# Performance work log

Measured on AMD Instinct MI355X. Metric: run time of the kernel, lower is better.

## Reference

```python
import jax, jax.numpy as jnp
import numpy as np

HIDDEN = 768
INTER = 2048
N_EXPERTS = 8
TOP_K = 2
SWIGLU_LIMIT = 7.0
N_TOK = 8192


def setup_inputs() -> dict:
    key = jax.random.key(0)
    k_x, k_r, k_gu, k_d = jax.random.split(key, 4)
    x = jax.random.normal(k_x, (N_TOK, HIDDEN), dtype=jnp.float32)
    router_w = jax.random.normal(k_r, (N_EXPERTS, HIDDEN), dtype=jnp.float32) * 0.02
    gate_up_proj = jax.random.normal(k_gu, (N_EXPERTS, 2 * INTER, HIDDEN), dtype=jnp.float32) * 0.02
    down_proj = jax.random.normal(k_d, (N_EXPERTS, HIDDEN, INTER), dtype=jnp.float32) * 0.02
    return {"x": x, "router_w": router_w, "gate_up_proj": gate_up_proj, "down_proj": down_proj}


def reference(x, router_w, gate_up_proj, down_proj):
    # router: [n_tok, E]
    router_logits = x @ router_w.T
    topk_vals, topk_idx = jax.lax.top_k(router_logits, TOP_K)  # [n_tok, k]
    topk_weights = jax.nn.softmax(topk_vals.astype(jnp.float32), axis=-1).astype(x.dtype)

    out = jnp.zeros_like(x)
    # Loop over the small fixed expert set; each expert is a dense GEMM over all
    # tokens, masked by its per-token routing weight (0 for unrouted tokens) —
    # identical math to the original gather/GEMM/scatter dispatch.
    for e in range(N_EXPERTS):
        # per-token weight for expert e (sums slots; each expert appears at most once per token)
        w_e = jnp.sum(jnp.where(topk_idx == e, topk_weights, 0.0), axis=-1)  # [n_tok]
        gate_up = x @ gate_up_proj[e].T  # [n_tok, 2*I]
        gate, up = jnp.split(gate_up, 2, axis=-1)
        up = jnp.minimum(up, SWIGLU_LIMIT)
        mlp_out = (jax.nn.silu(gate) * up) @ down_proj[e].T  # [n_tok, H]
        out = out + mlp_out * w_e[:, None]
    return out
```

## Files before the change

### kernel.cpp

```cpp
#include <hip/hip_runtime.h>
#include <hip/hip_bf16.h>

typedef unsigned short u16;
typedef unsigned int u32;
typedef short bf16x8 __attribute__((ext_vector_type(8)));
typedef float f32x4 __attribute__((ext_vector_type(4)));

#define NTOK 8192
#define HID 768
#define INTER 2048
#define NEXP 8

#define MFMA16(a, b, c) __builtin_amdgcn_mfma_f32_16x16x32_bf16(a, b, c, 0, 0, 0)
#define S_BARRIER() __builtin_amdgcn_s_barrier()
#define SETPRIO(x) __builtin_amdgcn_s_setprio(x)
#define WAITVM(n) asm volatile("s_waitcnt vmcnt(" #n ")" ::: "memory")

__device__ __forceinline__ u16 f2bf(float f) {
    u32 u = __builtin_bit_cast(u32, f);
    u32 r = (u + 0x7FFFu + ((u >> 16) & 1u)) >> 16;
    return (u16)r;
}

__device__ __forceinline__ void gld16(const void* g, void* l) {
    __builtin_amdgcn_global_load_lds((const __attribute__((address_space(1))) void*)g,
                                     (__attribute__((address_space(3))) void*)l, 16, 0, 0);
}

__global__ __launch_bounds__(256) void zero_kernel(float4* out4, int n4) {
    int i = blockIdx.x * blockDim.x + threadIdx.x;
    float4 z = {0.f, 0.f, 0.f, 0.f};
    int stride = gridDim.x * blockDim.x;
    for (int k = i; k < n4; k += stride) out4[k] = z;
}

__global__ __launch_bounds__(256) void cvt_kernel(const float* __restrict__ src, u16* __restrict__ dst, int n8) {
    int i = blockIdx.x * blockDim.x + threadIdx.x;
    int stride = gridDim.x * blockDim.x;
    for (; i < n8; i += stride) {
        const float4* s = (const float4*)(src + (size_t)i * 8);
        float4 a = s[0], b = s[1];
        u16 r[8] = {f2bf(a.x), f2bf(a.y), f2bf(a.z), f2bf(a.w),
                    f2bf(b.x), f2bf(b.y), f2bf(b.z), f2bf(b.w)};
        *(uint4*)(dst + (size_t)i * 8) = *(const uint4*)r;
    }
}

__global__ __launch_bounds__(256) void router2(const float* __restrict__ x, const float* __restrict__ rw,
                                               u32* __restrict__ route, float* __restrict__ wslot) {
    int wv = threadIdx.x >> 6, ln = threadIdx.x & 63;
    int t = blockIdx.x * 4 + wv;
    if (t >= NTOK) return;
    float xr[12];
#pragma unroll
    for (int j = 0; j < 12; j++) xr[j] = x[(size_t)t * HID + ln + j * 64];
    float lg[NEXP];
#pragma unroll
    for (int e = 0; e < NEXP; e++) {
        float a = 0.f;
#pragma unroll
        for (int j = 0; j < 12; j++) a += xr[j] * rw[e * HID + ln + j * 64];
#pragma unroll
        for (int off = 32; off; off >>= 1) a += __shfl_xor(a, off);
        lg[e] = a;
    }
    int i0 = 0;
    float v0 = lg[0];
#pragma unroll
    for (int e = 1; e < NEXP; e++)
        if (lg[e] > v0) { v0 = lg[e]; i0 = e; }
    int i1 = -1;
    float v1 = -1e30f;
#pragma unroll
    for (int e = 0; e < NEXP; e++) {
        if (e == i0) continue;
        if (lg[e] > v1) { v1 = lg[e]; i1 = e; }
    }
    float w0 = 1.f / (1.f + __expf(v1 - v0));
    float w1 = 1.f - w0;
    if (ln == 0) {
        wslot[0 * NTOK + t] = w0;
        wslot[1 * NTOK + t] = w1;
        route[t] = (u32)i0 | ((u32)i1 << 8);
    }
}

__global__ __launch_bounds__(1024) void scatter_kernel(const u32* __restrict__ route, int* __restrict__ counts,
                                                       int* __restrict__ tokslot, int* __restrict__ ntiles,
                                                       int* __restrict__ tiledesc) {
    __shared__ int sc[NEXP][1024];
    int tid = threadIdx.x;
    u32 rt[8];
    int cnt[NEXP] = {0, 0, 0, 0, 0, 0, 0, 0};
#pragma unroll
    for (int k = 0; k < 8; k++) {
        rt[k] = route[tid * 8 + k];
        cnt[rt[k] & 255]++;
        cnt[(rt[k] >> 8) & 255]++;
    }
#pragma unroll
    for (int e = 0; e < NEXP; e++) sc[e][tid] = cnt[e];
    __syncthreads();
    for (int off = 1; off < 1024; off <<= 1) {
        int v[NEXP];
#pragma unroll
        for (int e = 0; e < NEXP; e++) v[e] = (tid >= off) ? sc[e][tid - off] : 0;
        __syncthreads();
#pragma unroll
        for (int e = 0; e < NEXP; e++)
            if (tid >= off) sc[e][tid] += v[e];
        __syncthreads();
    }
    int base[NEXP];
#pragma unroll
    for (int e = 0; e < NEXP; e++) base[e] = sc[e][tid] - cnt[e];
#pragma unroll
    for (int k = 0; k < 8; k++) {
        int t = tid * 8 + k;
        int e0 = rt[k] & 255, e1 = (rt[k] >> 8) & 255;
        tokslot[e0 * NTOK + base[e0]] = t;
        base[e0]++;
        tokslot[e1 * NTOK + base[e1]] = t | (1 << 16);
        base[e1]++;
    }
    if (tid == 0) {
        int tot = 0;
        for (int e = 0; e < NEXP; e++) {
            int c = sc[e][1023];
            counts[e] = c;
            int nt = (c + 255) >> 8;
            for (int q = 0; q < nt; q++) tiledesc[tot++] = (e << 8) | q;
        }
        ntiles[0] = tot;
    }
}


#define STAGE4(d, kt)                                        \
    do {                                                     \
        char* dA_ = lds + (d)*32768 + tid * 16;              \
        char* dB_ = dA_ + 16384;                             \
        size_t ko_ = (size_t)(kt)*64;                        \
        gld16(aP[0] + ko_, dA_);                             \
        gld16(aP[1] + ko_, dA_ + 8192);                      \
        gld16(bP[0] + ko_, dB_);                             \
        gld16(bP[1] + ko_, dB_ + 8192);                      \
    } while (0)

#define MMALL()                                                           \
    do {                                                                  \
        _Pragma("unroll") for (int m_ = 0; m_ < 8; m_++)                  \
            _Pragma("unroll") for (int n_ = 0; n_ < 4; n_++)              \
                acc[m_][n_] = MFMA16(af[m_], bfr[n_], acc[m_][n_]);       \
    } while (0)

#define PIPE4(NKT)                                                        \
    f32x4 acc[8][4];                                                      \
    _Pragma("unroll") for (int m_ = 0; m_ < 8; m_++)                      \
        _Pragma("unroll") for (int n_ = 0; n_ < 4; n_++) acc[m_][n_] = (f32x4)0.f; \
    const int aBase = (wr * 128 + rsel) * 64;                             \
    const int bBase = 16384 + (wc * 64 + rsel) * 64;                      \
    const int sOff = ((g4 ^ (rsel & 3) ^ ((rsel >> 2) & 3)) << 4);        \
    STAGE4(0, 0);                                                         \
    STAGE4(1, 1);                                                         \
    STAGE4(2, 2);                                                         \
    WAITVM(8);                                                            \
    S_BARRIER();                                                          \
    for (int t = 0; t < (NKT); ++t) {                                     \
        if (t + 3 < (NKT)) STAGE4((t + 3) & 3, t + 3);                    \
        const char* Tb = lds + (t & 3) * 32768;                           \
        bf16x8 af[8], bfr[4];                                             \
        _Pragma("unroll") for (int m_ = 0; m_ < 8; m_++)                  \
            af[m_] = *(const bf16x8*)(Tb + aBase + m_ * 1024 + sOff);     \
        _Pragma("unroll") for (int n_ = 0; n_ < 4; n_++)                  \
            bfr[n_] = *(const bf16x8*)(Tb + bBase + n_ * 1024 + sOff);    \
        SETPRIO(1); MMALL(); SETPRIO(0);                                  \
        if (t < (NKT)-3) { WAITVM(8); S_BARRIER(); }                      \
        else if (t == (NKT)-3) { WAITVM(4); S_BARRIER(); }                \
        else if (t == (NKT)-2) { WAITVM(0); S_BARRIER(); }                \
    }

__global__ __launch_bounds__(512, 2) void gateup4p(const u16* __restrict__ xb, const u16* __restrict__ gub,
                                                   const int* __restrict__ counts,
                                                   const int* __restrict__ ntiles, const int* __restrict__ tiledesc,
                                                   const int* __restrict__ tokslot, u16* __restrict__ h) {
    if ((int)blockIdx.y >= ntiles[0]) return;
    int td = tiledesc[blockIdx.y];
    int e = td >> 8;
    int cnt = counts[e];
    int row0 = (td & 255) * 256;
    int c0 = blockIdx.x * 128;

    extern __shared__ char lds[];
    int tid = threadIdx.x;
    int wv = tid >> 6, ln = tid & 63;
    int wr = wv >> 2, wc = wv & 3;
    int rsel = ln & 15, g4 = ln >> 4;

    int srow = tid >> 2, sl = tid & 3;
    int sswz = ((sl ^ (srow & 3) ^ ((srow >> 2) & 3)) << 4);
    const char* aP[2];
    const char* bP[2];
#pragma unroll
    for (int c = 0; c < 2; c++) {
        int r = c * 128 + srow;
        int gr = row0 + r;
        gr = gr < cnt ? gr : cnt - 1;
        int tok = tokslot[e * NTOK + gr] & 0xFFFF;
        aP[c] = (const char*)xb + (size_t)tok * (HID * 2) + sswz;
        int wi = r & 63;
        int b = (wi >> 5) * 2048 + c0 + (r >> 6) * 32 + (wi & 31);
        bP[c] = (const char*)gub + ((size_t)e * 4096 + b) * (HID * 2) + sswz;
    }

    PIPE4(HID / 32)

#pragma unroll
    for (int mg = 0; mg < 8; mg++) {
#pragma unroll
        for (int j = 0; j < 4; j++) {
            int gr = row0 + wr * 128 + mg * 16 + g4 * 4 + j;
            if (gr >= cnt) continue;
            int ts = tokslot[e * NTOK + gr];
            int tok = ts & 0xFFFF, slot = ts >> 16;
            u16* hrow = h + (size_t)(slot * NTOK + tok) * INTER;
#pragma unroll
            for (int n = 0; n < 2; n++) {
                float gv = acc[mg][n][j];
                float uv = fminf(acc[mg][n + 2][j], 7.0f);
                float sg = gv / (1.0f + __expf(-gv));
                hrow[c0 + wc * 32 + n * 16 + rsel] = f2bf(sg * uv);
            }
        }
    }
}

__global__ __launch_bounds__(512, 2) void down4p(const u16* __restrict__ hb, const u16* __restrict__ dnb,
                                                 const int* __restrict__ counts,
                                                 const int* __restrict__ ntiles, const int* __restrict__ tiledesc,
                                                 const int* __restrict__ tokslot,
                                                 const float* __restrict__ wslot, float* __restrict__ out) {
    if ((int)blockIdx.y >= ntiles[0]) return;
    int td = tiledesc[blockIdx.y];
    int e = td >> 8;
    int cnt = counts[e];
    int row0 = (td & 255) * 256;
    int col0 = blockIdx.x * 256;

    extern __shared__ char lds[];
    int tid = threadIdx.x;
    int wv = tid >> 6, ln = tid & 63;
    int wr = wv >> 2, wc = wv & 3;
    int rsel = ln & 15, g4 = ln >> 4;

    int srow = tid >> 2, sl = tid & 3;
    int sswz = ((sl ^ (srow & 3) ^ ((srow >> 2) & 3)) << 4);
    const char* aP[2];
    const char* bP[2];
#pragma unroll
    for (int c = 0; c < 2; c++) {
        int r = c * 128 + srow;
        int gr = row0 + r;
        gr = gr < cnt ? gr : cnt - 1;
        int ts = tokslot[e * NTOK + gr];
        aP[c] = (const char*)hb + (size_t)((ts >> 16) * NTOK + (ts & 0xFFFF)) * (INTER * 2) + sswz;
        bP[c] = (const char*)dnb + ((size_t)e * HID + col0 + r) * (INTER * 2) + sswz;
    }

    PIPE4(INTER / 32)

#pragma unroll
    for (int mg = 0; mg < 8; mg++) {
#pragma unroll
        for (int j = 0; j < 4; j++) {
            int gr = row0 + wr * 128 + mg * 16 + g4 * 4 + j;
            if (gr >= cnt) continue;
            int ts = tokslot[e * NTOK + gr];
            int tok = ts & 0xFFFF, slot = ts >> 16;
            float w = wslot[slot * NTOK + tok];
#pragma unroll
            for (int n = 0; n < 4; n++) {
                int col = col0 + wc * 64 + n * 16 + rsel;
                atomicAdd(&out[(size_t)tok * HID + col], w * acc[mg][n][j]);
            }
        }
    }
}

extern "C" void kernel_launch(void* const* d_in, const int* in_sizes, int n_in,
                              void* d_out, int out_size, void* d_ws, size_t ws_size,
                              hipStream_t stream) {
    const float* x = (const float*)d_in[0];
    const float* rw = (const float*)d_in[1];
    const float* gu = (const float*)d_in[2];
    const float* dn = (const float*)d_in[3];
    float* out = (float*)d_out;
    char* ws = (char*)d_ws;

    int* counts = (int*)(ws + 0);
    int* ntiles = (int*)(ws + 64);
    int* tiledesc = (int*)(ws + 128);
    int* tokslot = (int*)(ws + 512);
    float* wslot = (float*)(ws + 262656);
    u16* xb = (u16*)(ws + 328192);
    u16* gub = (u16*)(ws + 12911104);
    u16* dnb = (u16*)(ws + 63242752);
    u16* hb = (u16*)(ws + 88408576);
    u32* route = (u32*)(ws + 88408576);

    zero_kernel<<<1024, 256, 0, stream>>>((float4*)out, NTOK * HID / 4);
    cvt_kernel<<<2048, 256, 0, stream>>>(x, xb, NTOK * HID / 8);
    cvt_kernel<<<2048, 256, 0, stream>>>(gu, gub, NEXP * 2 * INTER * HID / 8);
    cvt_kernel<<<2048, 256, 0, stream>>>(dn, dnb, NEXP * HID * INTER / 8);
    router2<<<NTOK / 4, 256, 0, stream>>>(x, rw, route, wslot);
    scatter_kernel<<<1, 1024, 0, stream>>>(route, counts, tokslot, ntiles, tiledesc);
    gateup4p<<<dim3(16, 72), 512, 131072, stream>>>(xb, gub, counts, ntiles, tiledesc, tokslot, hb);
    down4p<<<dim3(3, 72), 512, 131072, stream>>>(hb, dnb, counts, ntiles, tiledesc, tokslot, wslot, out);
}
```

Measured before the change: 333.3 us.

## Shrink GEMM blocks to 256 threads with double-buffered LDS pipeline

Both expert GEMM kernels move from 512-thread blocks with a 256x256 (down) or 256x128 (gate/up) tile and a 4-stage LDS ring to 256-thread blocks with 256x128 or 256x64 tiles and a 2-stage double buffer. The LDS footprint drops from 128KB to 48KB, so more blocks fit per CU and the grid doubles. The MFMA priority hints are removed, and the loop now waits on all outstanding loads every iteration. The risk is less global-to-LDS latency hiding and more redundant A-tile reloads across the extra column blocks.

```diff
diff --git a/kernel.cpp b/kernel.cpp
--- a/kernel.cpp
+++ b/kernel.cpp
@@ -13,7 +13,6 @@
 
 #define MFMA16(a, b, c) __builtin_amdgcn_mfma_f32_16x16x32_bf16(a, b, c, 0, 0, 0)
 #define S_BARRIER() __builtin_amdgcn_s_barrier()
-#define SETPRIO(x) __builtin_amdgcn_s_setprio(x)
 #define WAITVM(n) asm volatile("s_waitcnt vmcnt(" #n ")" ::: "memory")
 
 __device__ __forceinline__ u16 f2bf(float f) {
@@ -136,84 +135,80 @@
 }
 
 
-#define STAGE4(d, kt)                                        \
+#define STG(d, kt)                                           \
     do {                                                     \
-        char* dA_ = lds + (d)*32768 + tid * 16;              \
-        char* dB_ = dA_ + 16384;                             \
+        char* base_ = lds + (d)*24576 + (tid << 4);          \
         size_t ko_ = (size_t)(kt)*64;                        \
-        gld16(aP[0] + ko_, dA_);                             \
-        gld16(aP[1] + ko_, dA_ + 8192);                      \
-        gld16(bP[0] + ko_, dB_);                             \
-        gld16(bP[1] + ko_, dB_ + 8192);                      \
+        gld16(aP[0] + ko_, base_);                           \
+        gld16(aP[1] + ko_, base_ + 4096);                    \
+        gld16(aP[2] + ko_, base_ + 8192);                    \
+        gld16(aP[3] + ko_, base_ + 12288);                   \
+        gld16(bP[0] + ko_, base_ + 16384);                   \
+        gld16(bP[1] + ko_, base_ + 20480);                   \
     } while (0)
 
-#define MMALL()                                                           \
-    do {                                                                  \
+#define PIPE_MB(NKT)                                                      \
+    f32x4 acc[8][4];                                                      \
+    _Pragma("unroll") for (int m_ = 0; m_ < 8; m_++)                      \
+        _Pragma("unroll") for (int n_ = 0; n_ < 4; n_++) acc[m_][n_] = (f32x4)0.f; \
+    const int sOff = ((g4 ^ (rsel & 3) ^ ((rsel >> 2) & 3)) << 4);        \
+    const int aBase = (wr * 128 + rsel) * 64 + sOff;                      \
+    const int bBase = 16384 + (wc * 64 + rsel) * 64 + sOff;               \
+    STG(0, 0);                                                            \
+    WAITVM(0);                                                            \
+    S_BARRIER();                                                          \
+    for (int t = 0; t < (NKT); ++t) {                                     \
+        if (t + 1 < (NKT)) STG((t + 1) & 1, t + 1);                       \
+        const char* Tb = lds + (t & 1) * 24576;                           \
+        bf16x8 af[8], bfr[4];                                             \
+        _Pragma("unroll") for (int m_ = 0; m_ < 8; m_++)                  \
+            af[m_] = *(const bf16x8*)(Tb + aBase + m_ * 1024);            \
+        _Pragma("unroll") for (int n_ = 0; n_ < 4; n_++)                  \
+            bfr[n_] = *(const bf16x8*)(Tb + bBase + n_ * 1024);           \
         _Pragma("unroll") for (int m_ = 0; m_ < 8; m_++)                  \
             _Pragma("unroll") for (int n_ = 0; n_ < 4; n_++)              \
                 acc[m_][n_] = MFMA16(af[m_], bfr[n_], acc[m_][n_]);       \
-    } while (0)
-
-#define PIPE4(NKT)                                                        \
-    f32x4 acc[8][4];                                                      \
-    _Pragma("unroll") for (int m_ = 0; m_ < 8; m_++)                      \
-        _Pragma("unroll") for (int n_ = 0; n_ < 4; n_++) acc[m_][n_] = (f32x4)0.f; \
-    const int aBase = (wr * 128 + rsel) * 64;                             \
-    const int bBase = 16384 + (wc * 64 + rsel) * 64;                      \
-    const int sOff = ((g4 ^ (rsel & 3) ^ ((rsel >> 2) & 3)) << 4);        \
-    STAGE4(0, 0);                                                         \
-    STAGE4(1, 1);                                                         \
-    STAGE4(2, 2);                                                         \
-    WAITVM(8);                                                            \
-    S_BARRIER();                                                          \
-    for (int t = 0; t < (NKT); ++t) {                                     \
-        if (t + 3 < (NKT)) STAGE4((t + 3) & 3, t + 3);                    \
-        const char* Tb = lds + (t & 3) * 32768;                           \
-        bf16x8 af[8], bfr[4];                                             \
-        _Pragma("unroll") for (int m_ = 0; m_ < 8; m_++)                  \
-            af[m_] = *(const bf16x8*)(Tb + aBase + m_ * 1024 + sOff);     \
-        _Pragma("unroll") for (int n_ = 0; n_ < 4; n_++)                  \
-            bfr[n_] = *(const bf16x8*)(Tb + bBase + n_ * 1024 + sOff);    \
-        SETPRIO(1); MMALL(); SETPRIO(0);                                  \
-        if (t < (NKT)-3) { WAITVM(8); S_BARRIER(); }                      \
-        else if (t == (NKT)-3) { WAITVM(4); S_BARRIER(); }                \
-        else if (t == (NKT)-2) { WAITVM(0); S_BARRIER(); }                \
-    }
-
-__global__ __launch_bounds__(512, 2) void gateup4p(const u16* __restrict__ xb, const u16* __restrict__ gub,
-                                                   const int* __restrict__ counts,
-                                                   const int* __restrict__ ntiles, const int* __restrict__ tiledesc,
-                                                   const int* __restrict__ tokslot, u16* __restrict__ h) {
+        WAITVM(0);                                                        \
+        S_BARRIER();                                                      \
+    }
+
+__global__ __launch_bounds__(256, 2) void gateup_mb(const u16* __restrict__ xb, const u16* __restrict__ gub,
+                                                    const int* __restrict__ counts,
+                                                    const int* __restrict__ ntiles, const int* __restrict__ tiledesc,
+                                                    const int* __restrict__ tokslot, u16* __restrict__ h) {
     if ((int)blockIdx.y >= ntiles[0]) return;
     int td = tiledesc[blockIdx.y];
     int e = td >> 8;
     int cnt = counts[e];
     int row0 = (td & 255) * 256;
-    int c0 = blockIdx.x * 128;
+    int c0 = blockIdx.x * 64;
 
     extern __shared__ char lds[];
     int tid = threadIdx.x;
     int wv = tid >> 6, ln = tid & 63;
-    int wr = wv >> 2, wc = wv & 3;
+    int wr = wv >> 1, wc = wv & 1;
     int rsel = ln & 15, g4 = ln >> 4;
 
     int srow = tid >> 2, sl = tid & 3;
     int sswz = ((sl ^ (srow & 3) ^ ((srow >> 2) & 3)) << 4);
-    const char* aP[2];
+    const char* aP[4];
     const char* bP[2];
 #pragma unroll
-    for (int c = 0; c < 2; c++) {
-        int r = c * 128 + srow;
-        int gr = row0 + r;
+    for (int c = 0; c < 4; c++) {
+        int gr = row0 + c * 64 + srow;
         gr = gr < cnt ? gr : cnt - 1;
         int tok = tokslot[e * NTOK + gr] & 0xFFFF;
         aP[c] = (const char*)xb + (size_t)tok * (HID * 2) + sswz;
+    }
+#pragma unroll
+    for (int c = 0; c < 2; c++) {
+        int r = c * 64 + srow;
         int wi = r & 63;
         int b = (wi >> 5) * 2048 + c0 + (r >> 6) * 32 + (wi & 31);
         bP[c] = (const char*)gub + ((size_t)e * 4096 + b) * (HID * 2) + sswz;
     }
 
-    PIPE4(HID / 32)
+    PIPE_MB(HID / 32)
 
 #pragma unroll
     for (int mg = 0; mg < 8; mg++) {
@@ -235,39 +230,42 @@
     }
 }
 
-__global__ __launch_bounds__(512, 2) void down4p(const u16* __restrict__ hb, const u16* __restrict__ dnb,
-                                                 const int* __restrict__ counts,
-                                                 const int* __restrict__ ntiles, const int* __restrict__ tiledesc,
-                                                 const int* __restrict__ tokslot,
-                                                 const float* __restrict__ wslot, float* __restrict__ out) {
+__global__ __launch_bounds__(256, 2) void down_mb(const u16* __restrict__ hb, const u16* __restrict__ dnb,
+                                                  const int* __restrict__ counts,
+                                                  const int* __restrict__ ntiles, const int* __restrict__ tiledesc,
+                                                  const int* __restrict__ tokslot,
+                                                  const float* __restrict__ wslot, float* __restrict__ out) {
     if ((int)blockIdx.y >= ntiles[0]) return;
     int td = tiledesc[blockIdx.y];
     int e = td >> 8;
     int cnt = counts[e];
     int row0 = (td & 255) * 256;
-    int col0 = blockIdx.x * 256;
+    int col0 = blockIdx.x * 128;
 
     extern __shared__ char lds[];
     int tid = threadIdx.x;
     int wv = tid >> 6, ln = tid & 63;
-    int wr = wv >> 2, wc = wv & 3;
+    int wr = wv >> 1, wc = wv & 1;
     int rsel = ln & 15, g4 = ln >> 4;
 
     int srow = tid >> 2, sl = tid & 3;
     int sswz = ((sl ^ (srow & 3) ^ ((srow >> 2) & 3)) << 4);
-    const char* aP[2];
+    const char* aP[4];
     const char* bP[2];
 #pragma unroll
-    for (int c = 0; c < 2; c++) {
-        int r = c * 128 + srow;
-        int gr = row0 + r;
+    for (int c = 0; c < 4; c++) {
+        int gr = row0 + c * 64 + srow;
         gr = gr < cnt ? gr : cnt - 1;
         int ts = tokslot[e * NTOK + gr];
         aP[c] = (const char*)hb + (size_t)((ts >> 16) * NTOK + (ts & 0xFFFF)) * (INTER * 2) + sswz;
+    }
+#pragma unroll
+    for (int c = 0; c < 2; c++) {
+        int r = c * 64 + srow;
         bP[c] = (const char*)dnb + ((size_t)e * HID + col0 + r) * (INTER * 2) + sswz;
     }
 
-    PIPE4(INTER / 32)
+    PIPE_MB(INTER / 32)
 
 #pragma unroll
     for (int mg = 0; mg < 8; mg++) {
@@ -314,6 +312,6 @@
     cvt_kernel<<<2048, 256, 0, stream>>>(dn, dnb, NEXP * HID * INTER / 8);
     router2<<<NTOK / 4, 256, 0, stream>>>(x, rw, route, wslot);
     scatter_kernel<<<1, 1024, 0, stream>>>(route, counts, tokslot, ntiles, tiledesc);
-    gateup4p<<<dim3(16, 72), 512, 131072, stream>>>(xb, gub, counts, ntiles, tiledesc, tokslot, hb);
-    down4p<<<dim3(3, 72), 512, 131072, stream>>>(hb, dnb, counts, ntiles, tiledesc, tokslot, wslot, out);
-}
+    gateup_mb<<<dim3(32, 72), 256, 49152, stream>>>(xb, gub, counts, ntiles, tiledesc, tokslot, hb);
+    down_mb<<<dim3(6, 72), 256, 49152, stream>>>(hb, dnb, counts, ntiles, tiledesc, tokslot, wslot, out);
+}
```

After: 343.8 us. +3.2%, slower.
